# Performance work log

Measured on AMD Instinct MI355X. Metric: run time of the kernel, lower is better.

Reference implementation:

```python
import jax, jax.numpy as jnp
import numpy as np

NUM_GRAPHS = 16
NODES_PER = 1024
D = 128
H = 2
KPOS = 20
E = 262144


def _ln(x, g, b):
    mu = jnp.mean(x, axis=-1, keepdims=True)
    var = jnp.mean((x - mu) ** 2, axis=-1, keepdims=True)
    return (x - mu) * jax.lax.rsqrt(var + 1e-5) * g + b


def setup_inputs() -> dict:
    key = jax.random.key(0)
    ks = jax.random.split(key, 12)
    N = NUM_GRAPHS * NODES_PER
    s = 0.02
    return {
        "x": jax.random.normal(ks[0], (N, D), jnp.float32),
        "pos_enc": jax.random.normal(ks[1], (N, KPOS), jnp.float32),
        "pe_w": jax.random.normal(ks[2], (D, KPOS), jnp.float32) * s,
        "pe_b": jnp.zeros((D,), jnp.float32),
        "in_w": jax.random.normal(ks[3], (3 * D, D), jnp.float32) * s,
        "in_b": jnp.zeros((3 * D,), jnp.float32),
        "out_w": jax.random.normal(ks[4], (D, D), jnp.float32) * s,
        "out_b": jnp.zeros((D,), jnp.float32),
        "ln1_g": jnp.ones((D,), jnp.float32),
        "ln1_b": jnp.zeros((D,), jnp.float32),
        "ln2_g": jnp.ones((D,), jnp.float32),
        "ln2_b": jnp.zeros((D,), jnp.float32),
        "ff1_w": jax.random.normal(ks[5], (4 * D, D), jnp.float32) * s,
        "ff1_b": jnp.zeros((4 * D,), jnp.float32),
        "ff2_w": jax.random.normal(ks[6], (D, 4 * D), jnp.float32) * s,
        "ff2_b": jnp.zeros((D,), jnp.float32),
        "edge_index": jax.random.randint(ks[7], (2, E), 0, N, dtype=jnp.int32),
        "batch": jnp.repeat(jnp.arange(NUM_GRAPHS, dtype=jnp.int32), NODES_PER),
    }


def reference(x, pos_enc, pe_w, pe_b, in_w, in_b, out_w, out_b,
              ln1_g, ln1_b, ln2_g, ln2_b, ff1_w, ff1_b, ff2_w, ff2_b,
              edge_index, batch):
    # pos_enc Linear + add, then per-graph transformer (graphs equal-sized -> batched)
    h = x + pos_enc @ pe_w.T + pe_b  # (N, D)
    h = h.reshape(NUM_GRAPHS, NODES_PER, D)  # (B, S, D)

    hd = D // H
    qkv = h @ in_w.T + in_b  # (B, S, 3D)
    q, k, v = jnp.split(qkv, 3, axis=-1)

    def heads(t):
        return t.reshape(NUM_GRAPHS, NODES_PER, H, hd).transpose(0, 2, 1, 3)

    q, k, v = heads(q), heads(k), heads(v)  # (B, H, S, hd)
    scores = jnp.einsum('bhqd,bhkd->bhqk', q, k) / jnp.float32(np.sqrt(hd))
    attn = jax.nn.softmax(scores, axis=-1)
    ctx = jnp.einsum('bhqk,bhkd->bhqd', attn, v)
    ctx = ctx.transpose(0, 2, 1, 3).reshape(NUM_GRAPHS, NODES_PER, D)
    sa = ctx @ out_w.T + out_b

    # post-norm (PyTorch TransformerEncoderLayer default, eval mode: no dropout)
    h = _ln(h + sa, ln1_g, ln1_b)
    ff = jax.nn.relu(h @ ff1_w.T + ff1_b) @ ff2_w.T + ff2_b
    h = _ln(h + ff, ln2_g, ln2_b)
    return h.reshape(-1, D)
```

## Files before the change

### kernel.cpp

```cpp
#include <hip/hip_runtime.h>

typedef unsigned short u16;

#define NGRAPH 16
#define SEQ    1024
#define DIM    128
#define NHEAD  2
#define HDIM   64
#define KPOS   20
#define NTOT   (NGRAPH*SEQ)
#define QKVD   (3*DIM)

__device__ __forceinline__ float bf2f(u16 u) {
    return __uint_as_float(((unsigned int)u) << 16);
}
__device__ __forceinline__ u16 f2bf(float f) {
    unsigned int u = __float_as_uint(f);
    u += 0x7fffu + ((u >> 16) & 1u);
    return (u16)(u >> 16);
}

template<int CTRL>
__device__ __forceinline__ float dpp_ror(float x) {
    return __int_as_float(__builtin_amdgcn_update_dpp(
        __float_as_int(x), __float_as_int(x), CTRL, 0xF, 0xF, true));
}
__device__ __forceinline__ float row16_max(float x) {
    x = fmaxf(x, dpp_ror<0x121>(x));
    x = fmaxf(x, dpp_ror<0x122>(x));
    x = fmaxf(x, dpp_ror<0x124>(x));
    x = fmaxf(x, dpp_ror<0x128>(x));
    return x;
}
__device__ __forceinline__ float row16_sum(float x) {
    x += dpp_ror<0x121>(x);
    x += dpp_ror<0x122>(x);
    x += dpp_ror<0x124>(x);
    x += dpp_ror<0x128>(x);
    return x;
}

__device__ __forceinline__ float ld1(const void* p, int fbf, size_t i) {
    return fbf ? bf2f(((const u16*)p)[i]) : ((const float*)p)[i];
}
__device__ __forceinline__ float4 ldw8(const void* W, int fbf, size_t i) {
    if (fbf) return *(const float4*)((const u16*)W + i);
    const float* q = (const float*)W + i;
    float4 a = *(const float4*)q, b = *(const float4*)(q + 4);
    float4 r;
    u16* d = (u16*)&r;
    d[0]=f2bf(a.x); d[1]=f2bf(a.y); d[2]=f2bf(a.z); d[3]=f2bf(a.w);
    d[4]=f2bf(b.x); d[5]=f2bf(b.y); d[6]=f2bf(b.z); d[7]=f2bf(b.w);
    return r;
}

typedef __attribute__((ext_vector_type(8))) short bf16x8;
typedef __attribute__((ext_vector_type(4))) float f32x4;

__device__ __forceinline__ void gload16(const u16* g, u16* l) {
    __builtin_amdgcn_global_load_lds(
        (const __attribute__((address_space(1))) unsigned int*)(g),
        (__attribute__((address_space(3))) unsigned int*)(l), 16, 0, 0);
}
#define VMCNT0() asm volatile("s_waitcnt vmcnt(0)" ::: "memory")

__device__ __forceinline__ int detect_bf16(const u16* x) {
    int ok = 1;
    for (int i = 0; i < 256; i += 2) {
        unsigned e = (x[i] >> 7) & 0xFF;
        if (e < 60u || e > 180u) ok = 0;
    }
    return ok;
}
__global__ void detect_kernel(const u16* __restrict__ x, int* __restrict__ flag) {
    if (threadIdx.x == 0 && blockIdx.x == 0) *flag = detect_bf16(x);
}

__global__ __launch_bounds__(256)
void wconv_kernel(const void* __restrict__ in_w, const void* __restrict__ out_w,
                  const void* __restrict__ ff1_w, const void* __restrict__ ff2_w,
                  const u16* __restrict__ x,
                  u16* __restrict__ wbf, int* __restrict__ flag) {
    __shared__ int fsh;
    if (threadIdx.x == 0) {
        int ok = detect_bf16(x);
        fsh = ok;
        if (blockIdx.x == 0) *flag = ok;
    }
    __syncthreads();
    int fbf = fsh;
    int i8 = (blockIdx.x * 256 + threadIdx.x) * 8;
    const void* src; int off;
    if      (i8 <  49152) { src = in_w;  off = i8; }
    else if (i8 <  65536) { src = out_w; off = i8 - 49152; }
    else if (i8 < 131072) { src = ff1_w; off = i8 - 65536; }
    else                  { src = ff2_w; off = i8 - 131072; }
    *(float4*)&wbf[i8] = ldw8(src, fbf, off);
}

__global__ __launch_bounds__(256)
void pe_kernel(const void* __restrict__ x, const void* __restrict__ pos,
               const void* __restrict__ pe_w, const void* __restrict__ pe_b,
               u16* __restrict__ h0, const int* __restrict__ flag) {
    int fbf = *flag;
    __shared__ float wsh[DIM][KPOS + 1];
    int t = threadIdx.x;
    for (int i = t; i < DIM * KPOS; i += 256)
        wsh[i / KPOS][i % KPOS] = ld1(pe_w, fbf, i);
    __syncthreads();
    int row = blockIdx.x * 2 + (t >> 7), d = t & 127;
    float acc = 0.f;
#pragma unroll
    for (int k = 0; k < KPOS; ++k)
        acc += ld1(pos, fbf, (size_t)row * KPOS + k) * wsh[d][k];
    int rs = fbf ? 128 : 256;
    h0[(size_t)row * rs + d] =
        f2bf(ld1(x, fbf, (size_t)row * DIM + d) + acc + ld1(pe_b, fbf, d));
}

__global__ __launch_bounds__(256)
void qkvpe_kernel(const void* __restrict__ x, const void* __restrict__ pos,
                  const void* __restrict__ pe_w, const void* __restrict__ pe_b,
                  const u16* __restrict__ W, const void* __restrict__ bias,
                  u16* __restrict__ h0, u16* __restrict__ qkv,
                  u16* __restrict__ vt, const int* __restrict__ flag) {
    int fbf = *flag;
    int rs  = fbf ? 128 : 256;
    __shared__ __align__(16) u16 Ash[64][128];
    __shared__ __align__(16) u16 Wsh[2][128][128];
    __shared__ float wsh[DIM][KPOS + 1];
    __shared__ float possh[64][KPOS + 1];
    int t = threadIdx.x;
    int w = t >> 6, lane = t & 63, l16 = lane & 15, quad = lane >> 4;
    int n0 = blockIdx.x * 64;
    int xr = (l16 & 7) << 3;

#pragma unroll
    for (int i = 0; i < 8; ++i) {
        int r = w * 4 + i * 16 + (lane >> 4);
        int s = (lane & 15) ^ (r & 7);
        gload16(&W[(size_t)r * 128 + s * 8], &Wsh[0][w * 4 + i * 16][0]);
    }
    for (int i = t; i < DIM * KPOS; i += 256)
        wsh[i / KPOS][i % KPOS] = ld1(pe_w, fbf, i);
    for (int i = t; i < 64 * KPOS; i += 256)
        possh[i / KPOS][i % KPOS] =
            ld1(pos, fbf, (size_t)(n0 + i / KPOS) * KPOS + i % KPOS);
    asm volatile("s_waitcnt lgkmcnt(0)" ::: "memory");
    __builtin_amdgcn_s_barrier();

#pragma unroll
    for (int u = 0; u < 4; ++u) {
        int gu = t + u * 256;
        int r = gu >> 4, g = gu & 15;
        float4 hv;
        u16* hp = (u16*)&hv;
#pragma unroll
        for (int j = 0; j < 8; ++j) {
            int d = g * 8 + j;
            float a = ld1(x, fbf, (size_t)(n0 + r) * DIM + d) + ld1(pe_b, fbf, d);
#pragma unroll
            for (int k = 0; k < KPOS; ++k) a += possh[r][k] * wsh[d][k];
            hp[j] = f2bf(a);
        }
        *(float4*)&Ash[r][(g ^ (r & 7)) * 8] = hv;
        *(float4*)&h0[(size_t)(n0 + r) * rs + g * 8] = hv;
    }
    asm volatile("s_waitcnt lgkmcnt(0)" ::: "memory");
    __builtin_amdgcn_s_barrier();

#pragma unroll
    for (int m = 0; m < 3; ++m) {
        int m0 = m * 128;
        if (m < 2) {
#pragma unroll
            for (int i = 0; i < 8; ++i) {
                int r = w * 4 + i * 16 + (lane >> 4);
                int s = (lane & 15) ^ (r & 7);
                gload16(&W[(size_t)(m0 + 128 + r) * 128 + s * 8],
                        &Wsh[(m + 1) & 1][w * 4 + i * 16][0]);
            }
            asm volatile("s_waitcnt vmcnt(8)" ::: "memory");
        } else {
            asm volatile("s_waitcnt vmcnt(0)" ::: "memory");
        }
        __builtin_amdgcn_s_barrier();
        f32x4 acc[8] = {};
        __builtin_amdgcn_s_setprio(1);
#pragma unroll
        for (int kk = 0; kk < 4; ++kk) {
            bf16x8 af = *(const bf16x8*)&Ash[w * 16 + l16][(kk * 32 + quad * 8) ^ xr];
#pragma unroll
            for (int s = 0; s < 8; ++s) {
                bf16x8 bf = *(const bf16x8*)&Wsh[m & 1][s * 16 + l16][(kk * 32 + quad * 8) ^ xr];
                acc[s] = __builtin_amdgcn_mfma_f32_16x16x32_bf16(af, bf, acc[s], 0, 0, 0);
            }
        }
        __builtin_amdgcn_s_setprio(0);
        float bb[8];
#pragma unroll
        for (int s = 0; s < 8; ++s) bb[s] = ld1(bias, fbf, m0 + s * 16 + l16);
#pragma unroll
        for (int r = 0; r < 4; ++r) {
            int lr = w * 16 + quad * 4 + r;
            if (m == 2) {
                int n = n0 + lr;
                int bg = n >> 10, nl = n & 1023;
#pragma unroll
                for (int s = 0; s < 8; ++s)
                    vt[((size_t)(bg * 128) + s * 16 + l16) * SEQ + nl] =
                        f2bf(acc[s][r] + bb[s]);
            } else {
#pragma unroll
                for (int s = 0; s < 8; ++s)
                    qkv[(size_t)(n0 + lr) * QKVD + m0 + s * 16 + l16] =
                        f2bf(acc[s][r] + bb[s]);
            }
        }
        if (m < 2) __builtin_amdgcn_s_barrier();
    }
}

__global__ __launch_bounds__(256)
void attn2_kernel(const u16* __restrict__ qkv, const u16* __restrict__ vtp,
                  u16* __restrict__ ctx) {
    __shared__ __align__(16) u16 Qsh[64][72];
    __shared__ __align__(16) u16 Ksh[2][64][64];
    __shared__ __align__(16) u16 Vsh[2][64][64];
    __shared__ u16 Psh[64][72];
    int t    = threadIdx.x;
    int w    = t >> 6;
    int lane = t & 63;
    int l16  = lane & 15;
    int quad = lane >> 4;
    int xr   = (l16 & 7) << 3;
    int L = blockIdx.x;
    int ngh = gridDim.x >> 4;
    int qt, gh;
    if (ngh >= 8) {
        int g8 = L & 7; int rest = L >> 3;
        qt = rest & 15; gh = (rest >> 4) * 8 + g8;
    } else {
        qt = L & 15; gh = L >> 4;
    }
    int b = gh >> 1, h = gh & 1;

#pragma unroll
    for (int i = 0; i < 2; ++i) {
        int idx = t + i * 256;
        int r = idx >> 3, d8 = (idx & 7) * 8;
        size_t n = (size_t)b * SEQ + qt * 64 + r;
        float4 qv = *(const float4*)&qkv[n * QKVD + h * HDIM + d8];
        u16* qp = (u16*)&qv;
#pragma unroll
        for (int j = 0; j < 8; ++j) qp[j] = f2bf(bf2f(qp[j]) * 0.125f);
        *(float4*)&Qsh[r][d8] = qv;
    }

    const u16* kbase = qkv + (size_t)b * SEQ * QKVD + DIM + h * HDIM;
    const u16* vbase = vtp + (size_t)((b * 2 + h) * 64) * SEQ;

    auto stageKV = [&](int kt, int bf) {
#pragma unroll
        for (int i = 0; i < 2; ++i) {
            int r = w * 8 + i * 32 + (lane >> 3);
            int s = (lane & 7) ^ (r & 7);
            gload16(&kbase[(size_t)(kt * 64 + r) * QKVD + s * 8],
                    &Ksh[bf][w * 8 + i * 32][0]);
        }
#pragma unroll
        for (int i = 0; i < 2; ++i) {
            int r = w * 8 + i * 32 + (lane >> 3);
            int s = (lane & 7) ^ (r & 7);
            gload16(&vbase[(size_t)r * SEQ + kt * 64 + s * 8],
                    &Vsh[bf][w * 8 + i * 32][0]);
        }
    };

    stageKV(0, 0);
    VMCNT0();
    __syncthreads();
    bf16x8 qa0 = *(const bf16x8*)&Qsh[w * 16 + l16][quad * 8];
    bf16x8 qa1 = *(const bf16x8*)&Qsh[w * 16 + l16][32 + quad * 8];

    f32x4 o[4] = {};
    float mrow[4] = {-1e30f, -1e30f, -1e30f, -1e30f};
    float lrow[4] = {};

#pragma unroll 1
    for (int kt = 0; kt < SEQ / 64; ++kt) {
        int cur = kt & 1;
        if (kt + 1 < SEQ / 64) stageKV(kt + 1, cur ^ 1);

        float sc[4][4];
        __builtin_amdgcn_s_setprio(1);
#pragma unroll
        for (int c = 0; c < 4; ++c) {
            bf16x8 kb0 = *(const bf16x8*)&Ksh[cur][c * 16 + l16][(quad * 8) ^ xr];
            bf16x8 kb1 = *(const bf16x8*)&Ksh[cur][c * 16 + l16][(32 + quad * 8) ^ xr];
            f32x4 s = {};
            s = __builtin_amdgcn_mfma_f32_16x16x32_bf16(qa0, kb0, s, 0, 0, 0);
            s = __builtin_amdgcn_mfma_f32_16x16x32_bf16(qa1, kb1, s, 0, 0, 0);
#pragma unroll
            for (int r = 0; r < 4; ++r) sc[c][r] = s[r];
        }
        __builtin_amdgcn_s_setprio(0);
        float alpha[4];
#pragma unroll
        for (int r = 0; r < 4; ++r) {
            float mx = fmaxf(fmaxf(sc[0][r], sc[1][r]), fmaxf(sc[2][r], sc[3][r]));
            mx = row16_max(mx);
            float mnew = fmaxf(mrow[r], mx);
            alpha[r] = __expf(mrow[r] - mnew);
            mrow[r] = mnew;
            float sum = 0.f;
#pragma unroll
            for (int c = 0; c < 4; ++c) {
                float p = __expf(sc[c][r] - mnew);
                sc[c][r] = p;
                sum += p;
            }
            sum = row16_sum(sum);
            lrow[r] = lrow[r] * alpha[r] + sum;
        }
#pragma unroll
        for (int c = 0; c < 4; ++c)
#pragma unroll
            for (int r = 0; r < 4; ++r)
                Psh[w * 16 + quad * 4 + r][c * 16 + l16] = f2bf(sc[c][r]);
#pragma unroll
        for (int dt = 0; dt < 4; ++dt)
#pragma unroll
            for (int r = 0; r < 4; ++r) o[dt][r] *= alpha[r];
        bf16x8 pa0 = *(const bf16x8*)&Psh[w * 16 + l16][quad * 8];
        bf16x8 pa1 = *(const bf16x8*)&Psh[w * 16 + l16][32 + quad * 8];
        __builtin_amdgcn_s_setprio(1);
#pragma unroll
        for (int dt = 0; dt < 4; ++dt) {
            bf16x8 vb0 = *(const bf16x8*)&Vsh[cur][dt * 16 + l16][(quad * 8) ^ xr];
            bf16x8 vb1 = *(const bf16x8*)&Vsh[cur][dt * 16 + l16][(32 + quad * 8) ^ xr];
            o[dt] = __builtin_amdgcn_mfma_f32_16x16x32_bf16(pa0, vb0, o[dt], 0, 0, 0);
            o[dt] = __builtin_amdgcn_mfma_f32_16x16x32_bf16(pa1, vb1, o[dt], 0, 0, 0);
        }
        __builtin_amdgcn_s_setprio(0);
        if (kt + 1 < SEQ / 64) {
            VMCNT0();
            __syncthreads();
        }
    }
#pragma unroll
    for (int r = 0; r < 4; ++r) {
        float inv = 1.f / lrow[r];
        size_t n = (size_t)b * SEQ + qt * 64 + w * 16 + quad * 4 + r;
#pragma unroll
        for (int dt = 0; dt < 4; ++dt)
            ctx[n * DIM + h * HDIM + dt * 16 + l16] = f2bf(o[dt][r] * inv);
    }
}

__global__ __launch_bounds__(256)
void outffn_kernel(const u16* __restrict__ ctx, const u16* __restrict__ Wout,
                   const void* __restrict__ out_b,
                   const void* __restrict__ l1g, const void* __restrict__ l1b,
                   const u16* __restrict__ h0,
                   const u16* __restrict__ W1, const u16* __restrict__ W2,
                   const void* __restrict__ b1, const void* __restrict__ b2,
                   const void* __restrict__ l2g, const void* __restrict__ l2b,
                   void* __restrict__ outp, const int* __restrict__ flag) {
    int fbf = *flag;
    int rs  = fbf ? 128 : 256;
    __shared__ __align__(16) u16 Ash[64][128];
    __shared__ __align__(16) u16 Wsh[2][128][128];
    __shared__ __align__(16) u16 F1sh[4][64][128];
    u16 (*CtxSh)[128]  = (u16(*)[128])&F1sh[0][0][0];
    u16 (*WoutSh)[128] = (u16(*)[128])&F1sh[2][0][0];
    int t = threadIdx.x;
    int w = t >> 6, lane = t & 63, l16 = lane & 15, quad = lane >> 4;
    int n0 = blockIdx.x * 64;
    int xr = (l16 & 7) << 3;

#pragma unroll
    for (int i = 0; i < 4; ++i) {
        int r = w * 4 + i * 16 + (lane >> 4);
        int s = (lane & 15) ^ (r & 7);
        gload16(&ctx[(size_t)(n0 + r) * DIM + s * 8], &CtxSh[w * 4 + i * 16][0]);
    }
#pragma unroll
    for (int i = 0; i < 8; ++i) {
        int r = w * 4 + i * 16 + (lane >> 4);
        int s = (lane & 15) ^ (r & 7);
        gload16(&Wout[(size_t)r * 128 + s * 8], &WoutSh[w * 4 + i * 16][0]);
    }
#pragma unroll
    for (int i = 0; i < 8; ++i) {
        int r = w * 4 + i * 16 + (lane >> 4);
        int s = (lane & 15) ^ (r & 7);
        gload16(&W1[(size_t)r * 128 + s * 8], &Wsh[0][w * 4 + i * 16][0]);
    }
    asm volatile("s_waitcnt vmcnt(8)" ::: "memory");
    __builtin_amdgcn_s_barrier();

    {
        f32x4 acc[8] = {};
        __builtin_amdgcn_s_setprio(1);
#pragma unroll
        for (int kk = 0; kk < 4; ++kk) {
            bf16x8 af = *(const bf16x8*)&CtxSh[w * 16 + l16][(kk * 32 + quad * 8) ^ xr];
#pragma unroll
            for (int s = 0; s < 8; ++s) {
                bf16x8 bf = *(const bf16x8*)&WoutSh[s * 16 + l16][(kk * 32 + quad * 8) ^ xr];
                acc[s] = __builtin_amdgcn_mfma_f32_16x16x32_bf16(af, bf, acc[s], 0, 0, 0);
            }
        }
        __builtin_amdgcn_s_setprio(0);
        float bb[8], gg[8], be[8];
#pragma unroll
        for (int s = 0; s < 8; ++s) {
            bb[s] = ld1(out_b, fbf, s * 16 + l16);
            gg[s] = ld1(l1g, fbf, s * 16 + l16);
            be[s] = ld1(l1b, fbf, s * 16 + l16);
        }
#pragma unroll
        for (int r = 0; r < 4; ++r) {
            int lr = w * 16 + quad * 4 + r;
            size_t rg = (size_t)(n0 + lr);
            float v[8];
#pragma unroll
            for (int s = 0; s < 8; ++s)
                v[s] = acc[s][r] + bb[s] + bf2f(h0[rg * rs + s * 16 + l16]);
            float sm = 0.f, sq = 0.f;
#pragma unroll
            for (int s = 0; s < 8; ++s) { sm += v[s]; sq += v[s] * v[s]; }
            sm = row16_sum(sm);
            sq = row16_sum(sq);
            float mu  = sm * (1.f / DIM);
            float var = fmaxf(sq * (1.f / DIM) - mu * mu, 0.f);
            float rsq = rsqrtf(var + 1e-5f);
#pragma unroll
            for (int s = 0; s < 8; ++s) {
                int e = s * 16 + l16;
                int g = e >> 3;
                Ash[lr][((g ^ (lr & 7)) << 3) + (e & 7)] =
                    f2bf((v[s] - mu) * rsq * gg[s] + be[s]);
            }
        }
        asm volatile("s_waitcnt lgkmcnt(0)" ::: "memory");
        __builtin_amdgcn_s_barrier();
    }

#pragma unroll
    for (int m = 0; m < 4; ++m) {
#pragma unroll
        for (int i = 0; i < 8; ++i) {
            int r = w * 4 + i * 16 + (lane >> 4);
            int s = (lane & 15) ^ (r & 7);
            if (m < 3)
                gload16(&W1[(size_t)((m + 1) * 128 + r) * 128 + s * 8],
                        &Wsh[(m + 1) & 1][w * 4 + i * 16][0]);
            else
                gload16(&W2[(size_t)r * 512 + s * 8],
                        &Wsh[0][w * 4 + i * 16][0]);
        }
        asm volatile("s_waitcnt vmcnt(8)" ::: "memory");
        __builtin_amdgcn_s_barrier();
        f32x4 acc[8] = {};
        __builtin_amdgcn_s_setprio(1);
#pragma unroll
        for (int kk = 0; kk < 4; ++kk) {
            bf16x8 af = *(const bf16x8*)&Ash[w * 16 + l16][(kk * 32 + quad * 8) ^ xr];
#pragma unroll
            for (int s = 0; s < 8; ++s) {
                bf16x8 bf = *(const bf16x8*)&Wsh[m & 1][s * 16 + l16][(kk * 32 + quad * 8) ^ xr];
                acc[s] = __builtin_amdgcn_mfma_f32_16x16x32_bf16(af, bf, acc[s], 0, 0, 0);
            }
        }
        __builtin_amdgcn_s_setprio(0);
        float bb[8];
#pragma unroll
        for (int s = 0; s < 8; ++s) bb[s] = ld1(b1, fbf, m * 128 + s * 16 + l16);
#pragma unroll
        for (int r = 0; r < 4; ++r) {
            int lr = w * 16 + quad * 4 + r;
#pragma unroll
            for (int s = 0; s < 8; ++s) {
                int g = s * 2 + (l16 >> 3);
                F1sh[m][lr][((g ^ (lr & 7)) << 3) + (l16 & 7)] =
                    f2bf(fmaxf(acc[s][r] + bb[s], 0.f));
            }
        }
        asm volatile("s_waitcnt lgkmcnt(0)" ::: "memory");
        __builtin_amdgcn_s_barrier();
    }

    f32x4 acc2[8] = {};
#pragma unroll
    for (int c = 0; c < 4; ++c) {
        if (c < 3) {
#pragma unroll
            for (int i = 0; i < 8; ++i) {
                int r = w * 4 + i * 16 + (lane >> 4);
                int s = (lane & 15) ^ (r & 7);
                gload16(&W2[(size_t)r * 512 + (c + 1) * 128 + s * 8],
                        &Wsh[(c + 1) & 1][w * 4 + i * 16][0]);
            }
            asm volatile("s_waitcnt vmcnt(8)" ::: "memory");
        } else {
            asm volatile("s_waitcnt vmcnt(0)" ::: "memory");
        }
        __builtin_amdgcn_s_barrier();
        __builtin_amdgcn_s_setprio(1);
#pragma unroll
        for (int kk = 0; kk < 4; ++kk) {
            bf16x8 af = *(const bf16x8*)&F1sh[c][w * 16 + l16][(kk * 32 + quad * 8) ^ xr];
#pragma unroll
            for (int s = 0; s < 8; ++s) {
                bf16x8 bf = *(const bf16x8*)&Wsh[c & 1][s * 16 + l16][(kk * 32 + quad * 8) ^ xr];
                acc2[s] = __builtin_amdgcn_mfma_f32_16x16x32_bf16(af, bf, acc2[s], 0, 0, 0);
            }
        }
        __builtin_amdgcn_s_setprio(0);
        if (c < 3) __builtin_amdgcn_s_barrier();
    }

    float bb[8], gg[8], be[8];
#pragma unroll
    for (int s = 0; s < 8; ++s) {
        bb[s] = ld1(b2, fbf, s * 16 + l16);
        gg[s] = ld1(l2g, fbf, s * 16 + l16);
        be[s] = ld1(l2b, fbf, s * 16 + l16);
    }
#pragma unroll
    for (int r = 0; r < 4; ++r) {
        int lr = w * 16 + quad * 4 + r;
        size_t rg = (size_t)(n0 + lr);
        float v[8];
#pragma unroll
        for (int s = 0; s < 8; ++s) {
            int g = s * 2 + (l16 >> 3);
            float resid = bf2f(Ash[lr][((g ^ (lr & 7)) << 3) + (l16 & 7)]);
            v[s] = acc2[s][r] + bb[s] + resid;
        }
        float sm = 0.f, sq = 0.f;
#pragma unroll
        for (int s = 0; s < 8; ++s) { sm += v[s]; sq += v[s] * v[s]; }
        sm = row16_sum(sm);
        sq = row16_sum(sq);
        float mu  = sm * (1.f / DIM);
        float var = fmaxf(sq * (1.f / DIM) - mu * mu, 0.f);
        float rsq = rsqrtf(var + 1e-5f);
        if (fbf) {
            u16* o = (u16*)outp;
#pragma unroll
            for (int s = 0; s < 8; ++s)
                o[rg * 128 + s * 16 + l16] =
                    f2bf((v[s] - mu) * rsq * gg[s] + be[s]);
        } else {
            float* o = (float*)outp;
#pragma unroll
            for (int s = 0; s < 8; ++s)
                o[rg * 128 + s * 16 + l16] =
                    (v[s] - mu) * rsq * gg[s] + be[s];
        }
    }
}

template<int EPI, int NK>
__global__ __launch_bounds__(256)
void mgemm_kernel(const u16* __restrict__ A, const void* __restrict__ W,
                  int wbf16, const void* __restrict__ bias,
                  const u16* __restrict__ resid,
                  const void* __restrict__ lng, const void* __restrict__ lnb,
                  void* __restrict__ outp, u16* __restrict__ vt,
                  int Mtot, int AstrIn,
                  int arow0, int orow0, const int* __restrict__ flag) {
    const int K = NK * 128;
    int fbf  = *flag;
    int wfmt = wbf16 ? 1 : fbf;
    int rs   = fbf ? 128 : 256;
    int Astr = (AstrIn < 0) ? rs : AstrIn;
    __shared__ u16 Ash[64][136];
    __shared__ u16 Wsh[128][136];
    int t = threadIdx.x;
    int w = t >> 6, lane = t & 63, l16 = lane & 15, quad = lane >> 4;
    int n0 = blockIdx.x * 64;
    int m0 = blockIdx.y * 128;
    f32x4 acc[8] = {};
    float4 aR[4], wR[8];
#pragma unroll
    for (int i = 0; i < 4; ++i) {
        int idx = t + i * 256;
        int row = idx >> 4, k8 = (idx & 15) * 8;
        aR[i] = *(const float4*)&A[(size_t)(arow0 + n0 + row) * Astr + k8];
    }
#pragma unroll
    for (int i = 0; i < 8; ++i) {
        int idx = t + i * 256;
        int row = idx >> 4, k8 = (idx & 15) * 8;
        wR[i] = ldw8(W, wfmt, (size_t)(m0 + row) * K + k8);
    }
#pragma unroll 1
    for (int c = 0; c < NK; ++c) {
#pragma unroll
        for (int i = 0; i < 4; ++i) {
            int idx = t + i * 256;
            *(float4*)&Ash[idx >> 4][(idx & 15) * 8] = aR[i];
        }
#pragma unroll
        for (int i = 0; i < 8; ++i) {
            int idx = t + i * 256;
            *(float4*)&Wsh[idx >> 4][(idx & 15) * 8] = wR[i];
        }
        __syncthreads();
        if (c + 1 < NK) {
            int kc = (c + 1) * 128;
#pragma unroll
            for (int i = 0; i < 4; ++i) {
                int idx = t + i * 256;
                int row = idx >> 4, k8 = (idx & 15) * 8;
                aR[i] = *(const float4*)&A[(size_t)(arow0 + n0 + row) * Astr + kc + k8];
            }
#pragma unroll
            for (int i = 0; i < 8; ++i) {
                int idx = t + i * 256;
                int row = idx >> 4, k8 = (idx & 15) * 8;
                wR[i] = ldw8(W, wfmt, (size_t)(m0 + row) * K + kc + k8);
            }
        }
        __builtin_amdgcn_s_setprio(1);
#pragma unroll
        for (int kk = 0; kk < 4; ++kk) {
            bf16x8 af = *(const bf16x8*)&Ash[w * 16 + l16][kk * 32 + quad * 8];
#pragma unroll
            for (int s = 0; s < 8; ++s) {
                bf16x8 bf = *(const bf16x8*)&Wsh[s * 16 + l16][kk * 32 + quad * 8];
                acc[s] = __builtin_amdgcn_mfma_f32_16x16x32_bf16(af, bf, acc[s], 0, 0, 0);
            }
        }
        __builtin_amdgcn_s_setprio(0);
        if (c + 1 < NK) __syncthreads();
    }
    float bb[8];
#pragma unroll
    for (int s = 0; s < 8; ++s) bb[s] = ld1(bias, fbf, m0 + s * 16 + l16);
    float gg[8], be[8];
    if (EPI >= 2) {
#pragma unroll
        for (int s = 0; s < 8; ++s) {
            gg[s] = ld1(lng, fbf, s * 16 + l16);
            be[s] = ld1(lnb, fbf, s * 16 + l16);
        }
    }
#pragma unroll
    for (int r = 0; r < 4; ++r) {
        int lr = w * 16 + quad * 4 + r;
        float v[8];
#pragma unroll
        for (int s = 0; s < 8; ++s) {
            v[s] = acc[s][r] + bb[s];
            if (EPI == 1) v[s] = fmaxf(v[s], 0.f);
        }
        if (EPI <= 1) {
            u16* o = (u16*)outp;
#pragma unroll
            for (int s = 0; s < 8; ++s)
                o[(size_t)(n0 + lr) * Mtot + m0 + s * 16 + l16] = f2bf(v[s]);
        } else {
            size_t rg = (size_t)(orow0 + n0 + lr);
#pragma unroll
            for (int s = 0; s < 8; ++s)
                v[s] += bf2f(resid[rg * rs + s * 16 + l16]);
            float sm = 0.f, sq = 0.f;
#pragma unroll
            for (int s = 0; s < 8; ++s) { sm += v[s]; sq += v[s] * v[s]; }
            sm = row16_sum(sm);
            sq = row16_sum(sq);
            float mu  = sm * (1.f / DIM);
            float var = fmaxf(sq * (1.f / DIM) - mu * mu, 0.f);
            float rsq = rsqrtf(var + 1e-5f);
            if (EPI == 2) {
                u16* o = (u16*)outp;
#pragma unroll
                for (int s = 0; s < 8; ++s)
                    o[rg * rs + s * 16 + l16] =
                        f2bf((v[s] - mu) * rsq * gg[s] + be[s]);
            } else {
                if (fbf) {
                    u16* o = (u16*)outp;
#pragma unroll
                    for (int s = 0; s < 8; ++s)
                        o[rg * 128 + s * 16 + l16] =
                            f2bf((v[s] - mu) * rsq * gg[s] + be[s]);
                } else {
                    float* o = (float*)outp;
#pragma unroll
                    for (int s = 0; s < 8; ++s)
                        o[rg * 128 + s * 16 + l16] =
                            (v[s] - mu) * rsq * gg[s] + be[s];
                }
            }
        }
    }
}

__global__ __launch_bounds__(256)
void attn_lds_kernel(const u16* __restrict__ qkv, u16* __restrict__ ctx) {
    __shared__ u16 Qsh[64][72];
    __shared__ u16 Ksh[64][72];
    __shared__ u16 VshT[64][72];
    __shared__ u16 Psh[64][72];
    int t    = threadIdx.x;
    int w    = t >> 6;
    int lane = t & 63;
    int l16  = lane & 15;
    int quad = lane >> 4;
    int L = blockIdx.x;
    int qt = L & 15, gh = L >> 4;
    int b = gh >> 1, h = gh & 1;

#pragma unroll
    for (int i = 0; i < 2; ++i) {
        int idx = t + i * 256;
        int r = idx >> 3, d8 = (idx & 7) * 8;
        size_t n = (size_t)b * SEQ + qt * 64 + r;
        float4 qv = *(const float4*)&qkv[n * QKVD + h * HDIM + d8];
        u16* qp = (u16*)&qv;
#pragma unroll
        for (int j = 0; j < 8; ++j) qp[j] = f2bf(bf2f(qp[j]) * 0.125f);
        *(float4*)&Qsh[r][d8] = qv;
    }
    int kr = t >> 3, kd8 = (t & 7) * 8;
    int vr = t & 63, vdb = (t >> 6) * 16;
    float4 kR[2], vR[2];
    {
        size_t nk0 = (size_t)b * SEQ + kr;
        kR[0] = *(const float4*)&qkv[nk0 * QKVD + DIM + h * HDIM + kd8];
        kR[1] = *(const float4*)&qkv[(nk0 + 32) * QKVD + DIM + h * HDIM + kd8];
        size_t nv0 = (size_t)b * SEQ + vr;
        vR[0] = *(const float4*)&qkv[nv0 * QKVD + 2 * DIM + h * HDIM + vdb];
        vR[1] = *(const float4*)&qkv[nv0 * QKVD + 2 * DIM + h * HDIM + vdb + 8];
    }
    __syncthreads();
    bf16x8 qa0 = *(const bf16x8*)&Qsh[w * 16 + l16][quad * 8];
    bf16x8 qa1 = *(const bf16x8*)&Qsh[w * 16 + l16][32 + quad * 8];

    f32x4 o[4] = {};
    float mrow[4] = {-1e30f, -1e30f, -1e30f, -1e30f};
    float lrow[4] = {};

#pragma unroll 1
    for (int kt = 0; kt < SEQ / 64; ++kt) {
        *(float4*)&Ksh[kr][kd8]      = kR[0];
        *(float4*)&Ksh[kr + 32][kd8] = kR[1];
        {
            const u16* pa = (const u16*)&vR[0];
            const u16* pb = (const u16*)&vR[1];
#pragma unroll
            for (int j = 0; j < 8; ++j) VshT[vdb + j][vr] = pa[j];
#pragma unroll
            for (int j = 0; j < 8; ++j) VshT[vdb + 8 + j][vr] = pb[j];
        }
        __syncthreads();
        if (kt + 1 < SEQ / 64) {
            size_t nk0 = (size_t)b * SEQ + (kt + 1) * 64 + kr;
            kR[0] = *(const float4*)&qkv[nk0 * QKVD + DIM + h * HDIM + kd8];
            kR[1] = *(const float4*)&qkv[(nk0 + 32) * QKVD + DIM + h * HDIM + kd8];
            size_t nv0 = (size_t)b * SEQ + (kt + 1) * 64 + vr;
            vR[0] = *(const float4*)&qkv[nv0 * QKVD + 2 * DIM + h * HDIM + vdb];
            vR[1] = *(const float4*)&qkv[nv0 * QKVD + 2 * DIM + h * HDIM + vdb + 8];
        }
        float sc[4][4];
        __builtin_amdgcn_s_setprio(1);
#pragma unroll
        for (int c = 0; c < 4; ++c) {
            bf16x8 kb0 = *(const bf16x8*)&Ksh[c * 16 + l16][quad * 8];
            bf16x8 kb1 = *(const bf16x8*)&Ksh[c * 16 + l16][32 + quad * 8];
            f32x4 s = {};
            s = __builtin_amdgcn_mfma_f32_16x16x32_bf16(qa0, kb0, s, 0, 0, 0);
            s = __builtin_amdgcn_mfma_f32_16x16x32_bf16(qa1, kb1, s, 0, 0, 0);
#pragma unroll
            for (int r = 0; r < 4; ++r) sc[c][r] = s[r];
        }
        __builtin_amdgcn_s_setprio(0);
        float alpha[4];
#pragma unroll
        for (int r = 0; r < 4; ++r) {
            float mx = fmaxf(fmaxf(sc[0][r], sc[1][r]), fmaxf(sc[2][r], sc[3][r]));
            mx = row16_max(mx);
            float mnew = fmaxf(mrow[r], mx);
            alpha[r] = __expf(mrow[r] - mnew);
            mrow[r] = mnew;
            float sum = 0.f;
#pragma unroll
            for (int c = 0; c < 4; ++c) {
                float p = __expf(sc[c][r] - mnew);
                sc[c][r] = p;
                sum += p;
            }
            sum = row16_sum(sum);
            lrow[r] = lrow[r] * alpha[r] + sum;
        }
#pragma unroll
        for (int c = 0; c < 4; ++c)
#pragma unroll
            for (int r = 0; r < 4; ++r)
                Psh[w * 16 + quad * 4 + r][c * 16 + l16] = f2bf(sc[c][r]);
#pragma unroll
        for (int dt = 0; dt < 4; ++dt)
#pragma unroll
            for (int r = 0; r < 4; ++r) o[dt][r] *= alpha[r];
        bf16x8 pa0 = *(const bf16x8*)&Psh[w * 16 + l16][quad * 8];
        bf16x8 pa1 = *(const bf16x8*)&Psh[w * 16 + l16][32 + quad * 8];
        __builtin_amdgcn_s_setprio(1);
#pragma unroll
        for (int dt = 0; dt < 4; ++dt) {
            bf16x8 vb0 = *(const bf16x8*)&VshT[dt * 16 + l16][quad * 8];
            bf16x8 vb1 = *(const bf16x8*)&VshT[dt * 16 + l16][32 + quad * 8];
            o[dt] = __builtin_amdgcn_mfma_f32_16x16x32_bf16(pa0, vb0, o[dt], 0, 0, 0);
            o[dt] = __builtin_amdgcn_mfma_f32_16x16x32_bf16(pa1, vb1, o[dt], 0, 0, 0);
        }
        __builtin_amdgcn_s_setprio(0);
        __syncthreads();
    }
#pragma unroll
    for (int r = 0; r < 4; ++r) {
        float inv = 1.f / lrow[r];
        size_t n = (size_t)b * SEQ + qt * 64 + w * 16 + quad * 4 + r;
#pragma unroll
        for (int dt = 0; dt < 4; ++dt)
            ctx[n * DIM + h * HDIM + dt * 16 + l16] = f2bf(o[dt][r] * inv);
    }
}

extern "C" void kernel_launch(void* const* d_in, const int* in_sizes, int n_in,
                              void* d_out, int out_size, void* d_ws, size_t ws_size,
                              hipStream_t stream) {
    const void* x     = d_in[0];
    const void* pos   = d_in[1];
    const void* pe_w  = d_in[2];
    const void* pe_b  = d_in[3];
    const void* in_w  = d_in[4];
    const void* in_b  = d_in[5];
    const void* out_w = d_in[6];
    const void* out_b = d_in[7];
    const void* ln1_g = d_in[8];
    const void* ln1_b = d_in[9];
    const void* ln2_g = d_in[10];
    const void* ln2_b = d_in[11];
    const void* ff1_w = d_in[12];
    const void* ff1_b = d_in[13];
    const void* ff2_w = d_in[14];
    const void* ff2_b = d_in[15];

    char* wsb  = (char*)d_ws;
    int*  flag = (int*)(wsb + ((ws_size - 4) & ~(size_t)3));
    u16*  h01  = (u16*)d_out;
    const size_t MB = 1024 * 1024;

    if (ws_size >= 21 * MB) {
        u16* qkv = (u16*)wsb;
        u16* ctx = (u16*)(wsb + 12 * MB);
        u16* vt  = (u16*)(wsb + 16 * MB);
        u16* wbf = (u16*)(wsb + 20 * MB);
        u16* wb_in  = wbf;
        u16* wb_out = wbf + 49152;
        u16* wb_ff1 = wbf + 65536;
        u16* wb_ff2 = wbf + 131072;

        wconv_kernel<<<96, 256, 0, stream>>>(in_w, out_w, ff1_w, ff2_w,
                                             (const u16*)x, wbf, flag);
        qkvpe_kernel<<<NTOT / 64, 256, 0, stream>>>(
            x, pos, pe_w, pe_b, wb_in, in_b, h01, qkv, vt, flag);
        attn2_kernel<<<NGRAPH * NHEAD * 16, 256, 0, stream>>>(qkv, vt, ctx);
        outffn_kernel<<<NTOT / 64, 256, 0, stream>>>(
            ctx, wb_out, out_b, ln1_g, ln1_b, h01,
            wb_ff1, wb_ff2, ff1_b, ff2_b, ln2_g, ln2_b, d_out, flag);
    } else {
        u16* qkv_g = (u16*)wsb;
        u16* ctx_g = (u16*)(wsb + 768 * 1024);
        u16* f1_g  = (u16*)wsb;
        detect_kernel<<<1, 1, 0, stream>>>((const u16*)x, flag);
        pe_kernel<<<NTOT / 2, 256, 0, stream>>>(x, pos, pe_w, pe_b, h01, flag);
        for (int g = 0; g < NGRAPH; ++g) {
            int row0 = g * SEQ;
            mgemm_kernel<0,1><<<dim3(SEQ / 64, 3), 256, 0, stream>>>(
                h01, in_w, 0, in_b, nullptr, nullptr, nullptr, qkv_g, nullptr,
                QKVD, -1, row0, 0, flag);
            attn_lds_kernel<<<NHEAD * 16, 256, 0, stream>>>(qkv_g, ctx_g);
            mgemm_kernel<2,1><<<dim3(SEQ / 64, 1), 256, 0, stream>>>(
                ctx_g, out_w, 0, out_b, h01, ln1_g, ln1_b, h01, nullptr,
                DIM, DIM, 0, row0, flag);
        }
        for (int g = 0; g < NGRAPH; ++g) {
            int row0 = g * SEQ;
            mgemm_kernel<1,1><<<dim3(SEQ / 64, 4), 256, 0, stream>>>(
                h01, ff1_w, 0, ff1_b, nullptr, nullptr, nullptr, f1_g, nullptr,
                4 * DIM, -1, row0, 0, flag);
            mgemm_kernel<3,4><<<dim3(SEQ / 64, 1), 256, 0, stream>>>(
                f1_g, ff2_w, 0, ff2_b, h01, ln2_g, ln2_b, d_out, nullptr,
                DIM, 4 * DIM, 0, row0, flag);
        }
    }
}
```

Before: 172.9 us.

## Vectorize positional-encoding projection, stage residual via LDS, pad attention P buffer

The positional-encoding add is restructured so each thread loads x and pe_b with vector loads and reuses weight and pos values from LDS across four rows in a register-blocked FMA loop. The output/FFN kernel now stages the h0 residual into shared memory with async global-to-LDS loads, replacing scattered 2-byte global reads. The attention P buffer's row stride is padded to change LDS bank mapping. Costs are higher register pressure in the QKV kernel and extra LDS traffic and a larger vmcnt wait budget in the FFN kernel.

Measured after the change: 169.9 us (median of 2 runs). Within noise of the previous version (-1.7%).

```diff
diff --git a/kernel.cpp b/kernel.cpp
--- a/kernel.cpp
+++ b/kernel.cpp
@@ -52,6 +52,19 @@
     d[0]=f2bf(a.x); d[1]=f2bf(a.y); d[2]=f2bf(a.z); d[3]=f2bf(a.w);
     d[4]=f2bf(b.x); d[5]=f2bf(b.y); d[6]=f2bf(b.z); d[7]=f2bf(b.w);
     return r;
+}
+__device__ __forceinline__ void ld8f(const void* p, int fbf, size_t i, float* o) {
+    if (fbf) {
+        float4 v = *(const float4*)((const u16*)p + i);
+        const u16* q = (const u16*)&v;
+#pragma unroll
+        for (int j = 0; j < 8; ++j) o[j] = bf2f(q[j]);
+    } else {
+        float4 a = *(const float4*)((const float*)p + i);
+        float4 b = *(const float4*)((const float*)p + i + 4);
+        o[0]=a.x; o[1]=a.y; o[2]=a.z; o[3]=a.w;
+        o[4]=b.x; o[5]=b.y; o[6]=b.z; o[7]=b.w;
+    }
 }
 
 typedef __attribute__((ext_vector_type(8))) short bf16x8;
@@ -149,22 +162,41 @@
     asm volatile("s_waitcnt lgkmcnt(0)" ::: "memory");
     __builtin_amdgcn_s_barrier();
 
-#pragma unroll
-    for (int u = 0; u < 4; ++u) {
-        int gu = t + u * 256;
-        int r = gu >> 4, g = gu & 15;
-        float4 hv;
-        u16* hp = (u16*)&hv;
-#pragma unroll
-        for (int j = 0; j < 8; ++j) {
-            int d = g * 8 + j;
-            float a = ld1(x, fbf, (size_t)(n0 + r) * DIM + d) + ld1(pe_b, fbf, d);
-#pragma unroll
-            for (int k = 0; k < KPOS; ++k) a += possh[r][k] * wsh[d][k];
-            hp[j] = f2bf(a);
-        }
-        *(float4*)&Ash[r][(g ^ (r & 7)) * 8] = hv;
-        *(float4*)&h0[(size_t)(n0 + r) * rs + g * 8] = hv;
+    {
+        int g  = t & 15;
+        int r0 = t >> 4;
+        float acc[4][8];
+        float pb[8];
+        ld8f(pe_b, fbf, g * 8, pb);
+#pragma unroll
+        for (int u = 0; u < 4; ++u) {
+            int r = r0 + u * 16;
+            float xv[8];
+            ld8f(x, fbf, (size_t)(n0 + r) * DIM + g * 8, xv);
+#pragma unroll
+            for (int j = 0; j < 8; ++j) acc[u][j] = xv[j] + pb[j];
+        }
+#pragma unroll
+        for (int k = 0; k < KPOS; ++k) {
+            float wk[8], pk[4];
+#pragma unroll
+            for (int j = 0; j < 8; ++j) wk[j] = wsh[g * 8 + j][k];
+#pragma unroll
+            for (int u = 0; u < 4; ++u) pk[u] = possh[r0 + u * 16][k];
+#pragma unroll
+            for (int u = 0; u < 4; ++u)
+#pragma unroll
+                for (int j = 0; j < 8; ++j) acc[u][j] += pk[u] * wk[j];
+        }
+#pragma unroll
+        for (int u = 0; u < 4; ++u) {
+            int r = r0 + u * 16;
+            float4 hv; u16* hp = (u16*)&hv;
+#pragma unroll
+            for (int j = 0; j < 8; ++j) hp[j] = f2bf(acc[u][j]);
+            *(float4*)&Ash[r][(g ^ (r & 7)) * 8] = hv;
+            *(float4*)&h0[(size_t)(n0 + r) * rs + g * 8] = hv;
+        }
     }
     asm volatile("s_waitcnt lgkmcnt(0)" ::: "memory");
     __builtin_amdgcn_s_barrier();
@@ -227,7 +259,7 @@
     __shared__ __align__(16) u16 Qsh[64][72];
     __shared__ __align__(16) u16 Ksh[2][64][64];
     __shared__ __align__(16) u16 Vsh[2][64][64];
-    __shared__ u16 Psh[64][72];
+    __shared__ u16 Psh[64][76];
     int t    = threadIdx.x;
     int w    = t >> 6;
     int lane = t & 63;
@@ -373,6 +405,7 @@
     __shared__ __align__(16) u16 Wsh[2][128][128];
     __shared__ __align__(16) u16 F1sh[4][64][128];
     u16 (*CtxSh)[128]  = (u16(*)[128])&F1sh[0][0][0];
+    u16 (*H0Sh)[128]   = (u16(*)[128])&F1sh[1][0][0];
     u16 (*WoutSh)[128] = (u16(*)[128])&F1sh[2][0][0];
     int t = threadIdx.x;
     int w = t >> 6, lane = t & 63, l16 = lane & 15, quad = lane >> 4;
@@ -392,6 +425,12 @@
         gload16(&Wout[(size_t)r * 128 + s * 8], &WoutSh[w * 4 + i * 16][0]);
     }
 #pragma unroll
+    for (int i = 0; i < 4; ++i) {
+        int r = w * 4 + i * 16 + (lane >> 4);
+        int s = (lane & 15) ^ (r & 7);
+        gload16(&h0[(size_t)(n0 + r) * rs + s * 8], &H0Sh[w * 4 + i * 16][0]);
+    }
+#pragma unroll
     for (int i = 0; i < 8; ++i) {
         int r = w * 4 + i * 16 + (lane >> 4);
         int s = (lane & 15) ^ (r & 7);
@@ -423,11 +462,14 @@
 #pragma unroll
         for (int r = 0; r < 4; ++r) {
             int lr = w * 16 + quad * 4 + r;
-            size_t rg = (size_t)(n0 + lr);
             float v[8];
 #pragma unroll
-            for (int s = 0; s < 8; ++s)
-                v[s] = acc[s][r] + bb[s] + bf2f(h0[rg * rs + s * 16 + l16]);
+            for (int s = 0; s < 8; ++s) {
+                int e = s * 16 + l16;
+                int g = e >> 3;
+                float resid = bf2f(H0Sh[lr][((g ^ (lr & 7)) << 3) + (e & 7)]);
+                v[s] = acc[s][r] + bb[s] + resid;
+            }
             float sm = 0.f, sq = 0.f;
 #pragma unroll
             for (int s = 0; s < 8; ++s) { sm += v[s]; sq += v[s] * v[s]; }
```
